# Kernel tuning notes

Hardware: AMD Instinct MI355X
Metric: run time of the kernel (lower is better)

The kernel has to match this reference:

```python
import jax, jax.numpy as jnp
import numpy as np

BS, NCAM, CIN, H, W = 1, 6, 512, 32, 88
MID = 256
DBINS = 112  # (58 - 2) / 0.5
VX, VY, VZ = 128, 128, 16


def conv2d(x, w, pad=1):
    return jax.lax.conv_general_dilated(
        x, w, (1, 1), [(pad, pad), (pad, pad)],
        dimension_numbers=('NCHW', 'OIHW', 'NCHW'))


def grid_sample_3d(feat, grid):
    """F.grid_sample 3D, bilinear, padding_mode='zeros', align_corners=False.
    feat: (N, C, D, H, W); grid: (N, X, Y, Z, 3) with xyz -> (W, H, D) coords in [-1,1].
    Returns (N, C, X, Y, Z)."""
    N, C, D, Hh, Ww = feat.shape
    gx, gy, gz = grid[..., 0], grid[..., 1], grid[..., 2]
    ix = ((gx + 1.0) * Ww - 1.0) * 0.5
    iy = ((gy + 1.0) * Hh - 1.0) * 0.5
    iz = ((gz + 1.0) * D - 1.0) * 0.5
    ix0, iy0, iz0 = jnp.floor(ix), jnp.floor(iy), jnp.floor(iz)
    fx, fy, fz = ix - ix0, iy - iy0, iz - iz0
    feat_flat = feat.reshape(N, C, D * Hh * Ww)
    out = jnp.zeros((N, C) + grid.shape[1:-1], feat.dtype)
    for dz in (0, 1):
        for dy in (0, 1):
            for dx in (0, 1):
                xi, yi, zi = ix0 + dx, iy0 + dy, iz0 + dz
                w_ = ((fx if dx else 1.0 - fx) * (fy if dy else 1.0 - fy)
                      * (fz if dz else 1.0 - fz))
                valid = ((xi >= 0) & (xi < Ww) & (yi >= 0) & (yi < Hh)
                         & (zi >= 0) & (zi < D))
                xc = jnp.clip(xi, 0, Ww - 1).astype(jnp.int32)
                yc = jnp.clip(yi, 0, Hh - 1).astype(jnp.int32)
                zc = jnp.clip(zi, 0, D - 1).astype(jnp.int32)
                idx = ((zc * Hh + yc) * Ww + xc).reshape(N, 1, -1)
                g = jnp.take_along_axis(feat_flat, idx, axis=2)
                g = g.reshape((N, C) + grid.shape[1:-1])
                out = out + g * (w_ * valid)[:, None]
    return out


def setup_inputs():
    key = jax.random.key(0)
    ks = jax.random.split(key, 16)
    f32 = jnp.float32
    img_feat = jax.random.normal(ks[0], (BS, NCAM, CIN, H, W), f32)
    intr = np.zeros((NCAM, 4, 4), np.float32)
    for i in range(NCAM):
        f = 1266.0 + 10.0 * i
        intr[i, 0, 0] = f; intr[i, 1, 1] = f
        intr[i, 0, 2] = 800.0; intr[i, 1, 2] = 450.0
        intr[i, 2, 2] = 1.0; intr[i, 3, 3] = 1.0
    intrins = jnp.asarray(intr)[None]  # (1, 6, 4, 4)
    # normalized frustum-sample coords; slightly beyond [-1,1] to hit zero padding
    grid = jax.random.uniform(ks[1], (BS, NCAM, VX, VY, VZ, 3), f32, -1.1, 1.1)
    s3 = (2.0 / (CIN * 9)) ** 0.5
    sm = (2.0 / (MID * 9)) ** 0.5
    s1 = (2.0 / MID) ** 0.5
    red_w = jax.random.normal(ks[2], (MID, CIN, 3, 3), f32) * s3
    red_s = jnp.ones((MID,), f32); red_b = jnp.zeros((MID,), f32)
    mlp_w1 = jax.random.normal(ks[3], (1, MID), f32) * 1.4
    mlp_b1 = jnp.zeros((MID,), f32)
    mlp_w2 = jax.random.normal(ks[4], (MID, MID), f32) * s1
    mlp_b2 = jnp.zeros((MID,), f32)
    se_rw = jax.random.normal(ks[5], (MID, MID, 1, 1), f32) * s1
    se_rb = jnp.zeros((MID,), f32)
    se_ew = jax.random.normal(ks[6], (MID, MID, 1, 1), f32) * s1
    se_eb = jnp.zeros((MID,), f32)
    bb_w = jax.random.normal(ks[7], (3, 2, MID, MID, 3, 3), f32) * sm
    bb_s = jnp.ones((3, 2, MID), f32); bb_b = jnp.zeros((3, 2, MID), f32)
    dp_w = jax.random.normal(ks[8], (DBINS, MID, 1, 1), f32) * s1
    dp_b = jnp.zeros((DBINS,), f32)
    return dict(img_feat=img_feat, intrins=intrins, grid=grid,
                red_w=red_w, red_s=red_s, red_b=red_b,
                mlp_w1=mlp_w1, mlp_b1=mlp_b1, mlp_w2=mlp_w2, mlp_b2=mlp_b2,
                se_rw=se_rw, se_rb=se_rb, se_ew=se_ew, se_eb=se_eb,
                bb_w=bb_w, bb_s=bb_s, bb_b=bb_b, dp_w=dp_w, dp_b=dp_b)


def reference(img_feat, intrins, grid, red_w, red_s, red_b,
              mlp_w1, mlp_b1, mlp_w2, mlp_b2,
              se_rw, se_rb, se_ew, se_eb, bb_w, bb_s, bb_b, dp_w, dp_b):
    bs, n, c, h, w = img_feat.shape
    x = img_feat.reshape(bs * n, c, h, w)
    # pixel-size SE conditioning from inverse intrinsics
    inv = jnp.linalg.inv(intrins)
    pixel_size = jnp.linalg.norm(
        jnp.stack([inv[..., 0, 0], inv[..., 1, 1]], -1), axis=-1).reshape(-1, 1)
    sp = pixel_size * 1000.0  # scale_depth_factor
    # reduce_conv: conv3x3 + (folded) BN + ReLU
    x = conv2d(x, red_w)
    x = jax.nn.relu(x * red_s[:, None, None] + red_b[:, None, None])
    # Mlp on scaled pixel size
    x_se = jax.nn.relu(sp @ mlp_w1 + mlp_b1) @ mlp_w2 + mlp_b2
    x_se = x_se[:, :, None, None]
    # SELayer
    t = jax.nn.relu(conv2d(x_se, se_rw, pad=0) + se_rb[:, None, None])
    gate = jax.nn.sigmoid(conv2d(t, se_ew, pad=0) + se_eb[:, None, None])
    x = x * gate
    # 3 BasicBlocks (conv-bn-relu-conv-bn + residual, relu), BN folded (eval)
    for i in range(3):
        y = conv2d(x, bb_w[i, 0])
        y = jax.nn.relu(y * bb_s[i, 0][:, None, None] + bb_b[i, 0][:, None, None])
        y = conv2d(y, bb_w[i, 1])
        y = y * bb_s[i, 1][:, None, None] + bb_b[i, 1][:, None, None]
        x = jax.nn.relu(x + y)
    depth = conv2d(x, dp_w, pad=0) + dp_b[:, None, None]  # (bs*n, D, h, w)
    dp = jax.nn.softmax(depth, axis=1)
    # stack depth prob and ones so one grid_sample yields features AND voxel mask
    feat = jnp.stack([dp, jnp.ones_like(dp)], axis=1)  # (bs*n, 2, D, h, w)
    g = grid.reshape((bs * n,) + grid.shape[2:])       # (bs*n, X, Y, Z, 3)
    sampled = grid_sample_3d(feat, g)                  # (bs*n, 2, X, Y, Z)
    sampled = sampled.reshape((bs, n) + sampled.shape[1:]).sum(axis=1)
    agg, masks = sampled[:, :1], sampled[:, 1:]
    out = jnp.where(masks > 0, agg / jnp.where(masks > 0, masks, 1.0), agg)
    return out  # (bs, 1, X, Y, Z)
```

## Files before the change

kernel.cpp:

```cpp
#include <hip/hip_runtime.h>

typedef _Float16 f16;
typedef _Float16 f16x8 __attribute__((ext_vector_type(8)));
typedef _Float16 f16x4 __attribute__((ext_vector_type(4)));
typedef float f32x4 __attribute__((ext_vector_type(4)));

#define NCAM 6
#define CINF 512
#define MIDC 256
#define DB   112
#define HH   32
#define WW   88
#define PH   34
#define PW   90
#define NPOS (HH*WW)
#define PTILE 64
#define PT_PER_CAM 44

#define O_GATE   0L
#define O_WFRED  6144L
#define O_WFBB   2365440L
#define O_WFDP   9443328L
#define O_XP0    9508864L
#define O_X1     28309504L
#define O_DP     28309504L
#define O_X2     37709824L
#define O_X3     47110144L

__device__ __forceinline__ void gl_lds16(const void* g, void* l) {
  __builtin_amdgcn_global_load_lds((const __attribute__((address_space(1))) void*)g,
                                   (__attribute__((address_space(3))) void*)l, 16, 0, 0);
}

__device__ void wfrag_body(const float* __restrict__ src, const float* __restrict__ scale,
                           f16* __restrict__ dst, int TAPS, int CI, int CO_SRC,
                           long per, long total, int lbid, int nb) {
  long i = (long)lbid * 256 + threadIdx.x;
  long stride = (long)nb * 256;
  int KST = CI >> 5;
  for (; i < total; i += stride) {
    int conv = (int)(i / per);
    long rem = i - (long)conv * per;
    int j = (int)(rem & 7);
    int lane = (int)((rem >> 3) & 63);
    int mi = (int)((rem >> 9) & 3);
    long b = rem >> 11;
    int ks = (int)(b % KST);
    long b2 = b / KST;
    int tap = (int)(b2 % TAPS);
    int g = (int)(b2 / TAPS);
    int co = g * 64 + mi * 16 + (lane & 15);
    int ci = ks * 32 + (lane >> 4) * 8 + j;
    float v = 0.f;
    if (co < CO_SRC) {
      v = src[(long)conv * CO_SRC * CI * TAPS + ((long)co * CI + ci) * TAPS + tap];
      if (scale) v *= scale[conv * CO_SRC + co];
    }
    dst[i] = (f16)v;
  }
}

__global__ void prep_kernel(f16* __restrict__ xp0, f16* __restrict__ X1,
                            f16* __restrict__ X2, f16* __restrict__ X3,
                            const float* __restrict__ img,
                            const float* __restrict__ intr,
                            const float* __restrict__ w1, const float* __restrict__ b1,
                            const float* __restrict__ w2, const float* __restrict__ b2,
                            const float* __restrict__ rw, const float* __restrict__ rb,
                            const float* __restrict__ ew, const float* __restrict__ eb,
                            float* __restrict__ gate,
                            const float* __restrict__ red_w, const float* __restrict__ red_s,
                            f16* __restrict__ wfred,
                            const float* __restrict__ bb_w, const float* __restrict__ bb_s,
                            f16* __restrict__ wfbb,
                            const float* __restrict__ dp_w, f16* __restrict__ wfdp) {
  __shared__ float shbuf[1056];
  const int bid = blockIdx.x;
  if (bid < 915) {
    int idx = bid * 256 + threadIdx.x;
    f16* base; int C, rem;
    if (idx < 93696) { base = xp0; C = 512; rem = idx; }
    else {
      int k = idx - 93696;
      int bsel = k / 46848;
      if (bsel >= 3) return;
      rem = k - bsel * 46848; C = 256;
      base = (bsel == 0) ? X1 : (bsel == 1) ? X2 : X3;
    }
    int chunks = C >> 3;
    int cell = rem / chunks, cc = rem - cell * chunks;
    int cam = cell / 244, p = cell - cam * 244;
    int hh, ww;
    if (p < 90)       { hh = 0;  ww = p; }
    else if (p < 180) { hh = 33; ww = p - 90; }
    else { int q = p - 180; hh = 1 + (q >> 1); ww = (q & 1) * 89; }
    long o = ((long)(cam * PH + hh) * PW + ww) * C + cc * 8;
    f16x8 z = {0,0,0,0,0,0,0,0};
    *(f16x8*)(base + o) = z;
  } else if (bid < 10131) {
    int lb = bid - 915;
    int x = lb % 48;
    int h = (lb / 48) % 32;
    int n = lb / 1536;
    int wt = x % 3, ct = x / 3;
    float (*tile)[33] = (float(*)[33])shbuf;
    int tx = threadIdx.x & 31, ty = threadIdx.x >> 5;
    int w0 = wt * 32, c0 = ct * 32;
    #pragma unroll
    for (int i = 0; i < 4; ++i) {
      int cl = ty + i * 8;
      int w = w0 + tx;
      float v = 0.f;
      if (w < WW) v = img[((long)(n * CINF + c0 + cl) * HH + h) * WW + w];
      tile[cl][tx] = v;
    }
    __syncthreads();
    #pragma unroll
    for (int i = 0; i < 4; ++i) {
      int wl = ty + i * 8;
      int w = w0 + wl;
      if (w < WW)
        xp0[((long)((n * PH + h + 1) * PW + (w + 1))) * CINF + c0 + tx] = (f16)tile[tx][wl];
    }
  } else if (bid < 10137) {
    int n = bid - 10131, c = threadIdx.x;
    float* sps = shbuf;
    float* h1 = shbuf + 32;
    float* h2 = shbuf + 288;
    float* tt = shbuf + 544;
    if (c == 0) {
      float a[4][8];
      for (int i = 0; i < 4; ++i)
        for (int j = 0; j < 4; ++j) {
          a[i][j] = intr[n * 16 + i * 4 + j];
          a[i][4 + j] = (i == j) ? 1.f : 0.f;
        }
      for (int col = 0; col < 4; ++col) {
        int piv = col;
        for (int r2 = col + 1; r2 < 4; ++r2)
          if (fabsf(a[r2][col]) > fabsf(a[piv][col])) piv = r2;
        if (piv != col)
          for (int j = 0; j < 8; ++j) { float tv = a[col][j]; a[col][j] = a[piv][j]; a[piv][j] = tv; }
        float invp = 1.f / a[col][col];
        for (int j = 0; j < 8; ++j) a[col][j] *= invp;
        for (int r2 = 0; r2 < 4; ++r2)
          if (r2 != col) {
            float f = a[r2][col];
            for (int j = 0; j < 8; ++j) a[r2][j] -= f * a[col][j];
          }
      }
      float i00 = a[0][4], i11 = a[1][5];
      sps[0] = sqrtf(i00 * i00 + i11 * i11) * 1000.f;
    }
    __syncthreads();
    float sp = sps[0];
    h1[c] = fmaxf(sp * w1[c] + b1[c], 0.f);
    __syncthreads();
    float acc = b2[c];
    for (int j = 0; j < MIDC; ++j) acc += h1[j] * w2[j * MIDC + c];
    h2[c] = acc;
    __syncthreads();
    acc = rb[c];
    for (int j = 0; j < MIDC; ++j) acc += rw[c * MIDC + j] * h2[j];
    tt[c] = fmaxf(acc, 0.f);
    __syncthreads();
    acc = eb[c];
    for (int j = 0; j < MIDC; ++j) acc += ew[c * MIDC + j] * tt[j];
    gate[n * MIDC + c] = 1.f / (1.f + expf(-acc));
  } else if (bid < 12185) {
    long per = 4L * 9 * 16 * 2048;
    wfrag_body(red_w, red_s, wfred, 9, 512, 256, per, per, bid - 10137, 2048);
  } else if (bid < 16281) {
    long per = 4L * 9 * 8 * 2048;
    wfrag_body(bb_w, bb_s, wfbb, 9, 256, 256, per, 6 * per, bid - 12185, 4096);
  } else {
    long per = 2L * 1 * 8 * 2048;
    wfrag_body(dp_w, nullptr, wfdp, 1, 256, 112, per, per, bid - 16281, 128);
  }
}

template<int MODE, int CIN_T, int TAPS>
__global__ __launch_bounds__(256, 2)
void conv_mfma(const f16* __restrict__ X, const f16* __restrict__ Wf,
               const float* __restrict__ bias, const float* __restrict__ gate,
               const f16* __restrict__ res, f16* __restrict__ Yf16,
               float* __restrict__ Yf32, int co_tiles) {
  constexpr int KST = CIN_T / 32;
  constexpr int CPT = CIN_T / 64;
  constexpr int NCH = TAPS * CPT;
  constexpr int LCPT = (CPT == 8) ? 3 : 2;
  constexpr long GSTR = (long)TAPS * KST * 4096;
  __shared__ __align__(16) char S[49152];

  const int t = threadIdx.x;
  const int wv = t >> 6, ln = t & 63, lm = ln & 15, quad = ln >> 4;
  const int wm = wv >> 1, wn = wv & 1;
  const int bid0 = blockIdx.x;
  const int cpx = gridDim.x >> 3;
  const int bid = (bid0 & 7) * cpx + (bid0 >> 3);
  const int co_tile = bid % co_tiles;
  const int ptile = bid / co_tiles;
  const int cam = ptile / PT_PER_CAM;
  const int pbase = (ptile % PT_PER_CAM) * PTILE;

  const f16* gB[2]; int ldsoffB[2];
  const int clog = (ln & 7) ^ (ln >> 3);
  #pragma unroll
  for (int j = 0; j < 2; ++j) {
    int reg = j * 4 + wv;
    int r = reg * 8 + (ln >> 3);
    int pos = pbase + r;
    int hh = pos / WW, w2 = pos - hh * WW;
    gB[j] = X + ((long)((cam * PH + hh + 1) * PW + (w2 + 1))) * CIN_T + clog * 8;
    ldsoffB[j] = 16384 + reg * 1024;
  }

  const int base_l = (wn * 32 + lm) * 128;
  const int sx0 = ((0 * 4 + quad) ^ (lm & 7)) * 16;
  const int sx1 = ((1 * 4 + quad) ^ (lm & 7)) * 16;

  f32x4 acc[4][2];
  #pragma unroll
  for (int mi = 0; mi < 4; ++mi)
    #pragma unroll
    for (int ni = 0; ni < 2; ++ni)
      #pragma unroll
      for (int r = 0; r < 4; ++r) acc[mi][ni][r] = 0.f;

  auto choff = [&](int c) -> long {
    long off = 0;
    if (TAPS == 9) {
      int tp = c >> LCPT;
      int dy = tp / 3 - 1, dx = tp % 3 - 1;
      off = (long)(dy * PW + dx) * CIN_T;
    }
    return off + (long)(c & (CPT - 1)) * 64;
  };
  auto stageA = [&](int bsel, int c) {
    const char* sb = (const char*)Wf + (long)c * 8192 + (long)ln * 16;
    char* db = S + bsel * 24576;
    #pragma unroll
    for (int j = 0; j < 4; ++j) {
      int seg = j * 4 + wv;
      long gb = (long)(co_tile * 2 + (seg >> 3)) * GSTR;
      gl_lds16(sb + gb + (seg & 7) * 1024, db + seg * 1024);
    }
  };
  auto stageB = [&](int bsel, long curf) {
    #pragma unroll
    for (int j = 0; j < 2; ++j)
      gl_lds16(gB[j] + curf, S + bsel * 24576 + ldsoffB[j]);
  };
  auto compute = [&](int bsel) {
    const char* ab = S + bsel * 24576 + wm * 8192 + ln * 16;
    const char* bb = S + bsel * 24576 + 16384 + base_l;
    #pragma unroll
    for (int s = 0; s < 2; ++s) {
      f16x8 af[4];
      #pragma unroll
      for (int mi = 0; mi < 4; ++mi)
        af[mi] = *(const f16x8*)(ab + s * 4096 + mi * 1024);
      f16x8 bf[2];
      int sx = s ? sx1 : sx0;
      #pragma unroll
      for (int ni = 0; ni < 2; ++ni)
        bf[ni] = *(const f16x8*)(bb + ni * 2048 + sx);
      #pragma unroll
      for (int mi = 0; mi < 4; ++mi)
        #pragma unroll
        for (int ni = 0; ni < 2; ++ni)
          acc[mi][ni] = __builtin_amdgcn_mfma_f32_16x16x32_f16(af[mi], bf[ni], acc[mi][ni], 0, 0, 0);
    }
  };

  stageA(0, 0);
  stageB(0, choff(0));
  __syncthreads();

  #pragma unroll 1
  for (int c = 0; c < NCH; ++c) {
    int cur = c & 1;
    if (c + 1 < NCH) { stageA(cur ^ 1, c + 1); stageB(cur ^ 1, choff(c + 1)); }
    compute(cur);
    __syncthreads();
  }

  float4 b4[4], g4[4];
  bool skip[4];
  #pragma unroll
  for (int mi = 0; mi < 4; ++mi) {
    int co_l = wm * 64 + mi * 16 + quad * 4;
    int co_g = co_tile * 128 + co_l;
    skip[mi] = (MODE == 3) && (co_l >= DB);
    if (!skip[mi]) b4[mi] = *(const float4*)(bias + co_g);
    if (MODE == 0) g4[mi] = *(const float4*)(gate + cam * MIDC + co_g);
  }

  if (MODE == 3) {
    float* P = (float*)S;
    #pragma unroll
    for (int ni = 0; ni < 2; ++ni) {
      int prow = wn * 32 + ni * 16 + lm;
      #pragma unroll
      for (int mi = 0; mi < 4; ++mi) {
        if (skip[mi]) continue;
        int co_l = wm * 64 + mi * 16 + quad * 4;
        float4 o;
        o.x = acc[mi][ni][0] + ((float*)&b4[mi])[0];
        o.y = acc[mi][ni][1] + ((float*)&b4[mi])[1];
        o.z = acc[mi][ni][2] + ((float*)&b4[mi])[2];
        o.w = acc[mi][ni][3] + ((float*)&b4[mi])[3];
        *(float4*)(P + prow * 116 + co_l) = o;
      }
    }
    __syncthreads();
    int p = t >> 2, k = t & 3;
    const float* Pr = P + p * 116;
    float m = -1e30f;
    for (int b = k; b < DB; b += 4) m = fmaxf(m, Pr[b]);
    m = fmaxf(m, __shfl_xor(m, 1));
    m = fmaxf(m, __shfl_xor(m, 2));
    float e[28];
    float ssum = 0.f;
    int cnt = 0;
    for (int b = k; b < DB; b += 4) { float ev = __expf(Pr[b] - m); e[cnt++] = ev; ssum += ev; }
    ssum += __shfl_xor(ssum, 1);
    ssum += __shfl_xor(ssum, 2);
    float inv = 1.f / ssum;
    float* op = Yf32 + ((long)(cam * NPOS + pbase + p)) * DB;
    cnt = 0;
    for (int b = k; b < DB; b += 4) op[b] = e[cnt++] * inv;
    return;
  }

  #pragma unroll
  for (int ni = 0; ni < 2; ++ni) {
    int pos = pbase + wn * 32 + ni * 16 + lm;
    int hh = pos / WW, w2 = pos - hh * WW;
    long ob = ((long)((cam * PH + hh + 1) * PW + (w2 + 1))) * MIDC + co_tile * 128;
    #pragma unroll
    for (int mi = 0; mi < 4; ++mi) {
      int co_l = wm * 64 + mi * 16 + quad * 4;
      float v[4];
      #pragma unroll
      for (int r = 0; r < 4; ++r) {
        float y = acc[mi][ni][r];
        y += ((float*)&b4[mi])[r];
        if (MODE == 0) y = fmaxf(y, 0.f) * ((float*)&g4[mi])[r];
        else if (MODE == 1) y = fmaxf(y, 0.f);
        v[r] = y;
      }
      if (MODE == 2) {
        f16x4 rv = *(const f16x4*)(res + ob + co_l);
        f16x4 o;
        #pragma unroll
        for (int r = 0; r < 4; ++r) o[r] = (f16)fmaxf(v[r] + (float)rv[r], 0.f);
        *(f16x4*)(Yf16 + ob + co_l) = o;
      } else {
        f16x4 o;
        #pragma unroll
        for (int r = 0; r < 4; ++r) o[r] = (f16)v[r];
        *(f16x4*)(Yf16 + ob + co_l) = o;
      }
    }
  }
}

__global__ void sample_kernel(const float* __restrict__ grid, const float* __restrict__ dp,
                              float* __restrict__ out) {
  int v = blockIdx.x * blockDim.x + threadIdx.x;
  if (v >= 128 * 128 * 16) return;
  int vz = v & 15, vy = (v >> 4) & 127, vx = v >> 11;
  float agg = 0.f, msk = 0.f;
  #pragma unroll 1
  for (int n = 0; n < NCAM; ++n) {
    long gb = ((long)((n * 128 + vx) * 128 + vy) * 16 + vz) * 3;
    float gx = grid[gb], gy = grid[gb + 1], gz = grid[gb + 2];
    float ix = ((gx + 1.f) * (float)WW - 1.f) * 0.5f;
    float iy = ((gy + 1.f) * (float)HH - 1.f) * 0.5f;
    float iz = ((gz + 1.f) * (float)DB - 1.f) * 0.5f;
    float xf = floorf(ix), yf = floorf(iy), zf = floorf(iz);
    float fx = ix - xf, fy = iy - yf, fz = iz - zf;
    int x0 = (int)xf, y0 = (int)yf, z0 = (int)zf;
    float wxa[2] = {1.f - fx, fx};
    float wya[2] = {1.f - fy, fy};
    float wza[2] = {1.f - fz, fz};
    #pragma unroll
    for (int dy2 = 0; dy2 < 2; ++dy2) {
      int y = y0 + dy2;
      bool vyb = (y >= 0) && (y < HH);
      int yc = y < 0 ? 0 : (y > HH - 1 ? HH - 1 : y);
      #pragma unroll
      for (int dx2 = 0; dx2 < 2; ++dx2) {
        int x = x0 + dx2;
        bool vxb = (x >= 0) && (x < WW);
        int xc = x < 0 ? 0 : (x > WW - 1 ? WW - 1 : x);
        float wxy = wxa[dx2] * wya[dy2];
        const float* base = dp + ((long)((n * HH + yc) * WW + xc)) * DB;
        #pragma unroll
        for (int dz2 = 0; dz2 < 2; ++dz2) {
          int z = z0 + dz2;
          bool vzb = (z >= 0) && (z < DB);
          int zc = z < 0 ? 0 : (z > DB - 1 ? DB - 1 : z);
          float wgt = wxy * wza[dz2];
          if (vxb && vyb && vzb) {
            msk += wgt;
            agg += wgt * base[zc];
          }
        }
      }
    }
  }
  out[v] = (msk > 0.f) ? (agg / msk) : agg;
}

extern "C" void kernel_launch(void* const* d_in, const int* in_sizes, int n_in,
                              void* d_out, int out_size, void* d_ws, size_t ws_size,
                              hipStream_t stream) {
  const float* img   = (const float*)d_in[0];
  const float* intr  = (const float*)d_in[1];
  const float* grid  = (const float*)d_in[2];
  const float* red_w = (const float*)d_in[3];
  const float* red_s = (const float*)d_in[4];
  const float* red_b = (const float*)d_in[5];
  const float* w1    = (const float*)d_in[6];
  const float* b1    = (const float*)d_in[7];
  const float* w2    = (const float*)d_in[8];
  const float* b2    = (const float*)d_in[9];
  const float* rw    = (const float*)d_in[10];
  const float* rb    = (const float*)d_in[11];
  const float* ew    = (const float*)d_in[12];
  const float* eb    = (const float*)d_in[13];
  const float* bb_w  = (const float*)d_in[14];
  const float* bb_s  = (const float*)d_in[15];
  const float* bb_b  = (const float*)d_in[16];
  const float* dp_w  = (const float*)d_in[17];
  const float* dp_b  = (const float*)d_in[18];
  float* out = (float*)d_out;

  char* ws = (char*)d_ws;
  float* gate = (float*)(ws + O_GATE);
  f16* wfred  = (f16*)(ws + O_WFRED);
  f16* wfbb   = (f16*)(ws + O_WFBB);
  f16* wfdp   = (f16*)(ws + O_WFDP);
  f16* xp0    = (f16*)(ws + O_XP0);
  f16* X1     = (f16*)(ws + O_X1);
  f16* X2     = (f16*)(ws + O_X2);
  f16* X3     = (f16*)(ws + O_X3);
  float* dpb  = (float*)(ws + O_DP);

  prep_kernel<<<16409, 256, 0, stream>>>(xp0, X1, X2, X3, img,
                                         intr, w1, b1, w2, b2, rw, rb, ew, eb, gate,
                                         red_w, red_s, wfred, bb_w, bb_s, wfbb, dp_w, wfdp);

  const long WCH = 4L * 9 * 8 * 2048;

  conv_mfma<0, 512, 9><<<528, 256, 0, stream>>>(xp0, wfred, red_b, gate, nullptr, X1, nullptr, 2);

  conv_mfma<1, 256, 9><<<528, 256, 0, stream>>>(X1, wfbb + 0 * WCH, bb_b + 0 * 256, nullptr, nullptr, X2, nullptr, 2);
  conv_mfma<2, 256, 9><<<528, 256, 0, stream>>>(X2, wfbb + 1 * WCH, bb_b + 1 * 256, nullptr, X1, X3, nullptr, 2);
  conv_mfma<1, 256, 9><<<528, 256, 0, stream>>>(X3, wfbb + 2 * WCH, bb_b + 2 * 256, nullptr, nullptr, X2, nullptr, 2);
  conv_mfma<2, 256, 9><<<528, 256, 0, stream>>>(X2, wfbb + 3 * WCH, bb_b + 3 * 256, nullptr, X3, X1, nullptr, 2);
  conv_mfma<1, 256, 9><<<528, 256, 0, stream>>>(X1, wfbb + 4 * WCH, bb_b + 4 * 256, nullptr, nullptr, X2, nullptr, 2);
  conv_mfma<2, 256, 9><<<528, 256, 0, stream>>>(X2, wfbb + 5 * WCH, bb_b + 5 * 256, nullptr, X1, X3, nullptr, 2);

  conv_mfma<3, 256, 1><<<264, 256, 0, stream>>>(X3, wfdp, dp_b, nullptr, nullptr, nullptr, dpb, 1);

  sample_kernel<<<1024, 256, 0, stream>>>(grid, dpb, out);
}
```

Measured before the change: 462.3 us.

## Stage weight repacking through LDS per output-channel pair and branchless voxel sampling

Weight fragment packing now gives each block two output channels. The block loads their contiguous fp32 weights into shared memory with coalesced reads, then writes 16-byte f16x8 fragment chunks. This replaces the old per-element strided gather and scalar f16 stores. The sampling kernel hoists the clamp and validity computations, loads both z taps unconditionally with predicated weights, and unrolls the camera loop by two. Shared memory in the prep kernel grows to 36KB, which may lower occupancy for the other prep branches.

```diff
diff --git a/kernel.cpp b/kernel.cpp
--- a/kernel.cpp
+++ b/kernel.cpp
@@ -32,31 +32,46 @@
                                    (__attribute__((address_space(3))) void*)l, 16, 0, 0);
 }
 
-__device__ void wfrag_body(const float* __restrict__ src, const float* __restrict__ scale,
-                           f16* __restrict__ dst, int TAPS, int CI, int CO_SRC,
-                           long per, long total, int lbid, int nb) {
-  long i = (long)lbid * 256 + threadIdx.x;
-  long stride = (long)nb * 256;
-  int KST = CI >> 5;
-  for (; i < total; i += stride) {
-    int conv = (int)(i / per);
-    long rem = i - (long)conv * per;
-    int j = (int)(rem & 7);
-    int lane = (int)((rem >> 3) & 63);
-    int mi = (int)((rem >> 9) & 3);
-    long b = rem >> 11;
-    int ks = (int)(b % KST);
-    long b2 = b / KST;
-    int tap = (int)(b2 % TAPS);
-    int g = (int)(b2 / TAPS);
-    int co = g * 64 + mi * 16 + (lane & 15);
-    int ci = ks * 32 + (lane >> 4) * 8 + j;
+__device__ void wfrag_pair(const float* __restrict__ src, const float* __restrict__ scale,
+                           f16* __restrict__ dst, int TAPS, int CI, int CO_SRC, int G,
+                           long dstride, int lbid, float* __restrict__ W) {
+  const int pairs = G * 32;
+  const int pair = lbid % pairs;
+  const int conv = lbid / pairs;
+  const int co0 = pair * 2;
+  const int span1 = CI * TAPS;
+  const int span = 2 * span1;
+  const float* s0 = src + ((long)conv * CO_SRC + co0) * span1;
+  for (int i = threadIdx.x; i < span; i += 256) {
+    int co_rel = i / span1;
     float v = 0.f;
-    if (co < CO_SRC) {
-      v = src[(long)conv * CO_SRC * CI * TAPS + ((long)co * CI + ci) * TAPS + tap];
-      if (scale) v *= scale[conv * CO_SRC + co];
-    }
-    dst[i] = (f16)v;
+    if (co0 + co_rel < CO_SRC) v = s0[i];
+    W[i] = v;
+  }
+  __syncthreads();
+  const int KST = CI >> 5;
+  const int nchunk = 2 * TAPS * KST * 4;
+  float sc[2];
+  sc[0] = (scale && co0 < CO_SRC) ? scale[conv * CO_SRC + co0] : 1.f;
+  sc[1] = (scale && co0 + 1 < CO_SRC) ? scale[conv * CO_SRC + co0 + 1] : 1.f;
+  f16* db = dst + (long)conv * dstride;
+  for (int cnk = threadIdx.x; cnk < nchunk; cnk += 256) {
+    int quad = cnk & 3;
+    int b = cnk >> 2;
+    int ks = b % KST;
+    int b2 = b / KST;
+    int tap = b2 % TAPS;
+    int cosel = b2 / TAPS;
+    int co = co0 + cosel;
+    int g = co >> 6, mi = (co >> 4) & 3, lm = co & 15;
+    f16 tmp[8];
+    #pragma unroll
+    for (int j = 0; j < 8; ++j) {
+      int ci = ks * 32 + quad * 8 + j;
+      tmp[j] = (f16)(W[cosel * span1 + ci * TAPS + tap] * sc[cosel]);
+    }
+    long o = ((long)((g * TAPS + tap) * KST + ks) << 11) + (mi << 9) + ((quad * 16 + lm) << 3);
+    *(f16x8*)(db + o) = *(const f16x8*)tmp;
   }
 }
 
@@ -74,7 +89,7 @@
                             const float* __restrict__ bb_w, const float* __restrict__ bb_s,
                             f16* __restrict__ wfbb,
                             const float* __restrict__ dp_w, f16* __restrict__ wfdp) {
-  __shared__ float shbuf[1056];
+  __shared__ __align__(16) float shf[9216];
   const int bid = blockIdx.x;
   if (bid < 915) {
     int idx = bid * 256 + threadIdx.x;
@@ -103,7 +118,7 @@
     int h = (lb / 48) % 32;
     int n = lb / 1536;
     int wt = x % 3, ct = x / 3;
-    float (*tile)[33] = (float(*)[33])shbuf;
+    float (*tile)[33] = (float(*)[33])shf;
     int tx = threadIdx.x & 31, ty = threadIdx.x >> 5;
     int w0 = wt * 32, c0 = ct * 32;
     #pragma unroll
@@ -124,10 +139,10 @@
     }
   } else if (bid < 10137) {
     int n = bid - 10131, c = threadIdx.x;
-    float* sps = shbuf;
-    float* h1 = shbuf + 32;
-    float* h2 = shbuf + 288;
-    float* tt = shbuf + 544;
+    float* sps = shf;
+    float* h1 = shf + 32;
+    float* h2 = shf + 288;
+    float* tt = shf + 544;
     if (c == 0) {
       float a[4][8];
       for (int i = 0; i < 4; ++i)
@@ -167,15 +182,12 @@
     acc = eb[c];
     for (int j = 0; j < MIDC; ++j) acc += ew[c * MIDC + j] * tt[j];
     gate[n * MIDC + c] = 1.f / (1.f + expf(-acc));
-  } else if (bid < 12185) {
-    long per = 4L * 9 * 16 * 2048;
-    wfrag_body(red_w, red_s, wfred, 9, 512, 256, per, per, bid - 10137, 2048);
-  } else if (bid < 16281) {
-    long per = 4L * 9 * 8 * 2048;
-    wfrag_body(bb_w, bb_s, wfbb, 9, 256, 256, per, 6 * per, bid - 12185, 4096);
+  } else if (bid < 10265) {
+    wfrag_pair(red_w, red_s, wfred, 9, 512, 256, 4, 4L * 9 * 16 * 2048, bid - 10137, shf);
+  } else if (bid < 11033) {
+    wfrag_pair(bb_w, bb_s, wfbb, 9, 256, 256, 4, 4L * 9 * 8 * 2048, bid - 10265, shf);
   } else {
-    long per = 2L * 1 * 8 * 2048;
-    wfrag_body(dp_w, nullptr, wfdp, 1, 256, 112, per, per, bid - 16281, 128);
+    wfrag_pair(dp_w, nullptr, wfdp, 1, 256, 112, 2, 2L * 1 * 8 * 2048, bid - 11033, shf);
   }
 }
 
@@ -372,7 +384,7 @@
   if (v >= 128 * 128 * 16) return;
   int vz = v & 15, vy = (v >> 4) & 127, vx = v >> 11;
   float agg = 0.f, msk = 0.f;
-  #pragma unroll 1
+  #pragma unroll 2
   for (int n = 0; n < NCAM; ++n) {
     long gb = ((long)((n * 128 + vx) * 128 + vy) * 16 + vz) * 3;
     float gx = grid[gb], gy = grid[gb + 1], gz = grid[gb + 2];
@@ -382,32 +394,31 @@
     float xf = floorf(ix), yf = floorf(iy), zf = floorf(iz);
     float fx = ix - xf, fy = iy - yf, fz = iz - zf;
     int x0 = (int)xf, y0 = (int)yf, z0 = (int)zf;
-    float wxa[2] = {1.f - fx, fx};
-    float wya[2] = {1.f - fy, fy};
-    float wza[2] = {1.f - fz, fz};
+    const float* dpn = dp + (long)n * HH * WW * DB;
+    float wx[2] = {1.f - fx, fx};
+    float wy[2] = {1.f - fy, fy};
+    float wz[2] = {1.f - fz, fz};
+    int xc[2], yc[2], zc[2];
+    bool xv[2], yv[2], zv[2];
+    #pragma unroll
+    for (int d = 0; d < 2; ++d) {
+      int x = x0 + d; xv[d] = (x >= 0) && (x < WW); xc[d] = x < 0 ? 0 : (x > WW - 1 ? WW - 1 : x);
+      int y = y0 + d; yv[d] = (y >= 0) && (y < HH); yc[d] = y < 0 ? 0 : (y > HH - 1 ? HH - 1 : y);
+      int z = z0 + d; zv[d] = (z >= 0) && (z < DB); zc[d] = z < 0 ? 0 : (z > DB - 1 ? DB - 1 : z);
+    }
     #pragma unroll
     for (int dy2 = 0; dy2 < 2; ++dy2) {
-      int y = y0 + dy2;
-      bool vyb = (y >= 0) && (y < HH);
-      int yc = y < 0 ? 0 : (y > HH - 1 ? HH - 1 : y);
       #pragma unroll
       for (int dx2 = 0; dx2 < 2; ++dx2) {
-        int x = x0 + dx2;
-        bool vxb = (x >= 0) && (x < WW);
-        int xc = x < 0 ? 0 : (x > WW - 1 ? WW - 1 : x);
-        float wxy = wxa[dx2] * wya[dy2];
-        const float* base = dp + ((long)((n * HH + yc) * WW + xc)) * DB;
-        #pragma unroll
-        for (int dz2 = 0; dz2 < 2; ++dz2) {
-          int z = z0 + dz2;
-          bool vzb = (z >= 0) && (z < DB);
-          int zc = z < 0 ? 0 : (z > DB - 1 ? DB - 1 : z);
-          float wgt = wxy * wza[dz2];
-          if (vxb && vyb && vzb) {
-            msk += wgt;
-            agg += wgt * base[zc];
-          }
-        }
+        const float* base = dpn + ((long)(yc[dy2] * WW + xc[dx2])) * DB;
+        float d0 = base[zc[0]];
+        float d1 = base[zc[1]];
+        float wxy = wx[dx2] * wy[dy2];
+        bool vv = xv[dx2] && yv[dy2];
+        float w0 = (vv && zv[0]) ? wxy * wz[0] : 0.f;
+        float w1 = (vv && zv[1]) ? wxy * wz[1] : 0.f;
+        msk += w0 + w1;
+        agg += w0 * d0 + w1 * d1;
       }
     }
   }
@@ -449,7 +460,7 @@
   f16* X3     = (f16*)(ws + O_X3);
   float* dpb  = (float*)(ws + O_DP);
 
-  prep_kernel<<<16409, 256, 0, stream>>>(xp0, X1, X2, X3, img,
+  prep_kernel<<<11097, 256, 0, stream>>>(xp0, X1, X2, X3, img,
                                          intr, w1, b1, w2, b2, rw, rb, ew, eb, gate,
                                          red_w, red_s, wfred, bb_w, bb_s, wfbb, dp_w, wfdp);
 
```

Measured after the change: 459.6 us. About the same (-0.6%).
